# Kernel tuning notes

Hardware: AMD Instinct MI355X
Metric: run time of the kernel (lower is better)

## Reference

```python
import jax, jax.numpy as jnp
import numpy as np

B, T, E, H, C = 64, 512, 768, 128, 18


def setup_inputs() -> dict:
    key = jax.random.key(0)
    ks = jax.random.split(key, 16)
    s = 1.0 / np.sqrt(H)
    inp = {
        "x": jax.random.normal(ks[0], (B, T, E), jnp.float32),
        "attention_mask": jnp.ones((B, T), jnp.int32),
        "labels": jax.random.randint(ks[1], (B, T), 0, C, jnp.int32),
        "Wih_f": jax.random.uniform(ks[2], (4 * H, E), jnp.float32, -s, s),
        "Whh_f": jax.random.uniform(ks[3], (4 * H, H), jnp.float32, -s, s),
        "b_f": jax.random.uniform(ks[4], (4 * H,), jnp.float32, -s, s),
        "Wih_b": jax.random.uniform(ks[5], (4 * H, E), jnp.float32, -s, s),
        "Whh_b": jax.random.uniform(ks[6], (4 * H, H), jnp.float32, -s, s),
        "b_b": jax.random.uniform(ks[7], (4 * H,), jnp.float32, -s, s),
        "Wfc": jax.random.uniform(ks[8], (C, 2 * H), jnp.float32, -s, s),
        "bfc": jax.random.uniform(ks[9], (C,), jnp.float32, -s, s),
        "start_trans": jax.random.normal(ks[10], (C,), jnp.float32) * 0.1,
        "end_trans": jax.random.normal(ks[11], (C,), jnp.float32) * 0.1,
        "trans": jax.random.normal(ks[12], (C, C), jnp.float32) * 0.1,
    }
    return inp


def _lstm_dir(x, Wih, Whh, b, reverse=False):
    # x: [B, T, E] -> hidden states [B, T, H]; torch LSTM gate order i,f,g,o
    if reverse:
        x = x[:, ::-1]
    pre = jnp.einsum("bte,ge->btg", x, Wih) + b  # [B, T, 4H] input projection once
    h0 = jnp.zeros((x.shape[0], H), x.dtype)

    def step(carry, pt):
        h, c = carry
        g = pt + h @ Whh.T
        i, f, gg, o = jnp.split(g, 4, axis=-1)
        c = jax.nn.sigmoid(f) * c + jax.nn.sigmoid(i) * jnp.tanh(gg)
        h = jax.nn.sigmoid(o) * jnp.tanh(c)
        return (h, c), h

    _, hs = jax.lax.scan(step, (h0, h0), jnp.swapaxes(pre, 0, 1))
    hs = jnp.swapaxes(hs, 0, 1)
    if reverse:
        hs = hs[:, ::-1]
    return hs


def _crf_loglik(em, tags, mask, start, end, trans):
    # pytorch-crf log-likelihood, batch_first. em [B,T,C], tags/mask [B,T]
    b, t, _ = em.shape
    maskf = mask.astype(em.dtype)
    tags = tags.astype(jnp.int32)
    # numerator: score of the given tag path
    em_sc = jnp.take_along_axis(em, tags[..., None], axis=2)[..., 0]  # [B,T]
    num = start[tags[:, 0]] + em_sc[:, 0]
    num = num + jnp.sum(em_sc[:, 1:] * maskf[:, 1:], axis=1)
    num = num + jnp.sum(trans[tags[:, :-1], tags[:, 1:]] * maskf[:, 1:], axis=1)
    last_idx = jnp.sum(mask.astype(jnp.int32), axis=1) - 1
    last_tags = jnp.take_along_axis(tags, last_idx[:, None], axis=1)[:, 0]
    num = num + end[last_tags]
    # denominator: forward algorithm (logsumexp recurrence over time)
    alpha0 = start + em[:, 0]  # [B,C]

    def step(alpha, inp):
        e_t, m_t = inp
        new = jax.scipy.special.logsumexp(alpha[:, :, None] + trans[None], axis=1) + e_t
        return jnp.where(m_t[:, None], new, alpha), None

    alpha, _ = jax.lax.scan(
        step, alpha0,
        (jnp.swapaxes(em[:, 1:], 0, 1), jnp.swapaxes(mask[:, 1:].astype(bool), 0, 1)),
    )
    den = jax.scipy.special.logsumexp(alpha + end, axis=1)
    return num - den


def _viterbi(em, start, end, trans):
    # em [B,T,C] -> best path [B,T] (full mask)
    s0 = start + em[:, 0]

    def fstep(score, e_t):
        cand = score[:, :, None] + trans[None]  # [B,C,C]
        return jnp.max(cand, axis=1) + e_t, jnp.argmax(cand, axis=1)

    score, bptr = jax.lax.scan(fstep, s0, jnp.swapaxes(em[:, 1:], 0, 1))  # bptr [T-1,B,C]
    last = jnp.argmax(score + end, axis=1)  # [B]

    def bstep(tag, ptr_t):
        prev = jnp.take_along_axis(ptr_t, tag[:, None], axis=1)[:, 0]
        return prev, prev

    _, path = jax.lax.scan(bstep, last, bptr, reverse=True)  # [T-1,B]
    return jnp.concatenate([jnp.swapaxes(path, 0, 1), last[:, None]], axis=1)


def reference(x, attention_mask, labels, Wih_f, Whh_f, b_f, Wih_b, Whh_b, b_b,
              Wfc, bfc, start_trans, end_trans, trans):
    hf = _lstm_dir(x, Wih_f, Whh_f, b_f, reverse=False)
    hb = _lstm_dir(x, Wih_b, Whh_b, b_b, reverse=True)
    seq = jnp.concatenate([hf, hb], axis=-1)  # [B,T,2H]
    em = seq @ Wfc.T + bfc  # [B,T,C] emissions
    mask = attention_mask.astype(bool)
    llh = _crf_loglik(em, labels, mask, start_trans, end_trans, trans)
    loss = -jnp.sum(llh) / x.shape[0]  # reduction='sum' then / batch_size
    path = _viterbi(em, start_trans, end_trans, trans) + 1  # res_paths = x+1
    return path, loss
```

## Files before the change

### kernel.cpp

```cpp
#include <hip/hip_runtime.h>
#include <hip/hip_bf16.h>
#include <math.h>

typedef __attribute__((ext_vector_type(8))) short short8;
typedef __attribute__((ext_vector_type(4))) float f32x4;

constexpr int nB = 64, nT = 512, nE = 768, nH = 128, nG = 512, nC = 18;
constexpr int nBT = nB * nT;

__device__ __forceinline__ float bf2f(unsigned short u) { return __uint_as_float(((unsigned int)u) << 16); }
__device__ __forceinline__ unsigned short f2bf(float f) {
  __hip_bfloat16 h = __float2bfloat16(f);
  return *reinterpret_cast<unsigned short*>(&h);
}
__device__ __forceinline__ float rlane(float v, int lane) {
  return __uint_as_float(__builtin_amdgcn_readlane(__float_as_uint(v), lane));
}
__device__ __forceinline__ float fast_sig(float x) {
  return __builtin_amdgcn_rcpf(1.0f + __builtin_amdgcn_exp2f(-1.44269504f * x));
}
__device__ __forceinline__ float fast_tanh(float x) {
  return 1.0f - 2.0f * __builtin_amdgcn_rcpf(1.0f + __builtin_amdgcn_exp2f(2.88539008f * x));
}
__device__ __forceinline__ float max3h(float a, float b, float c) { return fmaxf(fmaxf(a, b), c); }

__global__ __launch_bounds__(256) void cvt_all(const float* __restrict__ x,
                                               const float* __restrict__ wF,
                                               const float* __restrict__ wB,
                                               unsigned short* __restrict__ xo,
                                               unsigned short* __restrict__ wFo,
                                               unsigned short* __restrict__ wBo) {
  const float* in; unsigned short* out; int n8, bid, nblk;
  if (blockIdx.x < 4096)      { in = x;  out = xo;  n8 = nBT * nE / 8; bid = blockIdx.x;        nblk = 4096; }
  else if (blockIdx.x < 4288) { in = wF; out = wFo; n8 = nG * nE / 8;  bid = blockIdx.x - 4096; nblk = 192; }
  else                        { in = wB; out = wBo; n8 = nG * nE / 8;  bid = blockIdx.x - 4288; nblk = 192; }
  int i = bid * 256 + threadIdx.x;
  const int stride = nblk * 256;
  for (; i < n8; i += stride) {
    const float4 a = ((const float4*)in)[(size_t)i * 2];
    const float4 b = ((const float4*)in)[(size_t)i * 2 + 1];
    unsigned short u[8] = {f2bf(a.x), f2bf(a.y), f2bf(a.z), f2bf(a.w),
                           f2bf(b.x), f2bf(b.y), f2bf(b.z), f2bf(b.w)};
    ((float4*)out)[i] = *(float4*)u;
  }
}

__global__ __launch_bounds__(256) void proj_kernel(
    const unsigned short* __restrict__ xbf,
    const unsigned short* __restrict__ wfb, const unsigned short* __restrict__ wbb,
    const float* __restrict__ biasF, const float* __restrict__ biasB,
    unsigned short* __restrict__ Pf, unsigned short* __restrict__ Pb)
{
  const int bid = blockIdx.x;
  const int mt = bid & 255, sub = bid >> 8;
  const int dir = sub >> 2, nt = sub & 3;
  const unsigned short* W = dir ? wbb : wfb;
  const float* bias = dir ? biasB : biasF;
  unsigned short* P = dir ? Pb : Pf;
  const int m0 = mt * 128, n0 = nt * 128;

  __shared__ unsigned short As[128 * 40];
  __shared__ unsigned short Bs[128 * 40];
  const int tid = threadIdx.x;
  const int w = tid >> 6, lane = tid & 63, l15 = lane & 15, l4 = lane >> 4;
  const int wr = w >> 1, wc = w & 1;
  const int srow = tid >> 1, shalf = tid & 1;

  const unsigned short* srcA = xbf + (size_t)(m0 + srow) * nE + shalf * 16;
  const unsigned short* srcB = W + (size_t)(n0 + srow) * nE + shalf * 16;

  f32x4 acc[4][4];
#pragma unroll
  for (int i = 0; i < 4; ++i)
#pragma unroll
    for (int j = 0; j < 4; ++j) acc[i][j] = (f32x4){0.f, 0.f, 0.f, 0.f};

  for (int k0 = 0; k0 < nE; k0 += 32) {
    const float4 a0 = *(const float4*)(srcA + k0);
    const float4 a1 = *(const float4*)(srcA + k0 + 8);
    const float4 b0 = *(const float4*)(srcB + k0);
    const float4 b1 = *(const float4*)(srcB + k0 + 8);
    __syncthreads();
    *(float4*)&As[srow * 40 + shalf * 16] = a0;
    *(float4*)&As[srow * 40 + shalf * 16 + 8] = a1;
    *(float4*)&Bs[srow * 40 + shalf * 16] = b0;
    *(float4*)&Bs[srow * 40 + shalf * 16 + 8] = b1;
    __syncthreads();
    short8 af[4], bfr[4];
#pragma unroll
    for (int i = 0; i < 4; ++i) af[i] = *(const short8*)&As[(wr * 64 + i * 16 + l15) * 40 + l4 * 8];
#pragma unroll
    for (int j = 0; j < 4; ++j) bfr[j] = *(const short8*)&Bs[(wc * 64 + j * 16 + l15) * 40 + l4 * 8];
#pragma unroll
    for (int i = 0; i < 4; ++i)
#pragma unroll
      for (int j = 0; j < 4; ++j)
        acc[i][j] = __builtin_amdgcn_mfma_f32_16x16x32_bf16(af[i], bfr[j], acc[i][j], 0, 0, 0);
  }
  float bv[4];
#pragma unroll
  for (int j = 0; j < 4; ++j) bv[j] = bias[n0 + wc * 64 + j * 16 + l15];
#pragma unroll
  for (int i = 0; i < 4; ++i) {
#pragma unroll
    for (int j = 0; j < 4; ++j) {
      const int col = n0 + wc * 64 + j * 16 + l15;
#pragma unroll
      for (int r = 0; r < 4; ++r) {
        const int row = m0 + wr * 64 + i * 16 + l4 * 4 + r;
        P[(size_t)row * nG + col] = f2bf(acc[i][j][r] + bv[j]);
      }
    }
  }
}

__global__ __launch_bounds__(256, 1) void lstm_kernel(
    const unsigned short* __restrict__ Pf, const unsigned short* __restrict__ Pb,
    const float* __restrict__ WhhF, const float* __restrict__ WhhB,
    unsigned short* __restrict__ hf, unsigned short* __restrict__ hb)
{
  const int bid = blockIdx.x;
  const int dir = bid & 1, pair = bid >> 1;
  const int b0 = pair * 2;
  const unsigned short* pre = dir ? Pb : Pf;
  const float* Whh = dir ? WhhB : WhhF;
  unsigned short* hout = dir ? hb : hf;

  const int tid = threadIdx.x, w = tid >> 6, lane = tid & 63;
  const int l15 = lane & 15, l4 = lane >> 4;
  const int batch = l15 & 1, msel = l15 >> 1;
  const int cell = w * 32 + msel * 4 + l4;

  __shared__ unsigned short h_lds[2 * 2 * 128];

  short8 Af[8][4];
#pragma unroll
  for (int m = 0; m < 8; ++m) {
    const int gp = w * 128 + m * 16 + l15;
    const int gorig = (gp & 3) * 128 + (gp >> 2);
#pragma unroll
    for (int kk = 0; kk < 4; ++kk) {
      const float* wp = Whh + (size_t)gorig * nH + kk * 32 + l4 * 8;
      const float4 v0 = *(const float4*)wp;
      const float4 v1 = *(const float4*)(wp + 4);
      unsigned short u[8] = {f2bf(v0.x), f2bf(v0.y), f2bf(v0.z), f2bf(v0.w),
                             f2bf(v1.x), f2bf(v1.y), f2bf(v1.z), f2bf(v1.w)};
      Af[m][kk] = *(short8*)u;
    }
  }
  for (int i = tid; i < 2 * 2 * 128; i += 256) h_lds[i] = 0;

  float c_state = 0.f;
  const unsigned short* pbase = pre + (size_t)(b0 + batch) * nT * nG + cell;

  unsigned short pA[4], pB[4];
  {
    const int tt0 = dir ? (nT - 1) : 0;
    const int tt1 = dir ? (nT - 2) : 1;
#pragma unroll
    for (int r = 0; r < 4; ++r) pA[r] = pbase[(size_t)tt0 * nG + r * 128];
#pragma unroll
    for (int r = 0; r < 4; ++r) pB[r] = pbase[(size_t)tt1 * nG + r * 128];
  }
  __syncthreads();

#define LSTM_STEP(RB, T, BUFC)                                                   \
  {                                                                              \
    const int ttime = dir ? (nT - 1 - (T)) : (T);                                \
    float pg[4];                                                                 \
    _Pragma("unroll")                                                            \
    for (int r = 0; r < 4; ++r) pg[r] = bf2f(BUFC[r]);                           \
    {                                                                            \
      const int tl = ((T) + 2 < nT) ? (T) + 2 : (T);                             \
      const int ttl = dir ? (nT - 1 - tl) : tl;                                  \
      _Pragma("unroll")                                                          \
      for (int r = 0; r < 4; ++r) BUFC[r] = pbase[(size_t)ttl * nG + r * 128];   \
    }                                                                            \
    short8 bfr[4];                                                               \
    _Pragma("unroll")                                                            \
    for (int kk = 0; kk < 4; ++kk)                                               \
      bfr[kk] = *(const short8*)&h_lds[(RB) * 256 + batch * 128 + kk * 32 + l4 * 8]; \
    f32x4 acc[8];                                                                \
    _Pragma("unroll")                                                            \
    for (int m = 0; m < 8; ++m) acc[m] = (f32x4){0.f, 0.f, 0.f, 0.f};            \
    _Pragma("unroll")                                                            \
    for (int kk = 0; kk < 4; ++kk)                                               \
      _Pragma("unroll")                                                          \
      for (int m = 0; m < 8; ++m)                                                \
        acc[m] = __builtin_amdgcn_mfma_f32_16x16x32_bf16(Af[m][kk], bfr[kk], acc[m], 0, 0, 0); \
    const f32x4 t0 = (msel & 1) ? acc[1] : acc[0];                               \
    const f32x4 t1 = (msel & 1) ? acc[3] : acc[2];                               \
    const f32x4 t2 = (msel & 1) ? acc[5] : acc[4];                               \
    const f32x4 t3 = (msel & 1) ? acc[7] : acc[6];                               \
    const f32x4 u0 = (msel & 2) ? t1 : t0;                                       \
    const f32x4 u1 = (msel & 2) ? t3 : t2;                                       \
    const f32x4 g = (msel & 4) ? u1 : u0;                                        \
    const float gi = g[0] + pg[0], gf = g[1] + pg[1], gg = g[2] + pg[2], go = g[3] + pg[3]; \
    c_state = fast_sig(gf) * c_state + fast_sig(gi) * fast_tanh(gg);             \
    const float hval = fast_sig(go) * fast_tanh(c_state);                        \
    const unsigned short hu = f2bf(hval);                                        \
    h_lds[((RB) ^ 1) * 256 + batch * 128 + cell] = hu;                           \
    hout[((size_t)(b0 + batch) * nT + ttime) * nH + cell] = hu;                  \
    asm volatile("s_waitcnt lgkmcnt(0)" ::: "memory");                           \
    __builtin_amdgcn_sched_barrier(0);                                           \
    __builtin_amdgcn_s_barrier();                                                \
  }

  for (int t2 = 0; t2 < nT; t2 += 2) {
    LSTM_STEP(0, t2, pA)
    LSTM_STEP(1, t2 + 1, pB)
  }
#undef LSTM_STEP
}

__global__ __launch_bounds__(256) void em_kernel(
    const unsigned short* __restrict__ hf, const unsigned short* __restrict__ hb,
    const float* __restrict__ Wfc, const float* __restrict__ bfc,
    float* __restrict__ em)
{
  __shared__ float seq[32][260];
  __shared__ float Wf[18][260];
  const int tid = threadIdx.x;
  const int row0 = blockIdx.x * 32;
  for (int i = tid; i < 32 * 32; i += 256) {
    const int r = i >> 5, seg = i & 31;
    const unsigned short* src = (seg < 16) ? (hf + (size_t)(row0 + r) * nH + seg * 8)
                                           : (hb + (size_t)(row0 + r) * nH + (seg - 16) * 8);
    const float4 v = *(const float4*)src;
    const unsigned short* u = (const unsigned short*)&v;
#pragma unroll
    for (int k = 0; k < 8; ++k) seq[r][seg * 8 + k] = bf2f(u[k]);
  }
  for (int i = tid; i < nC * 256; i += 256) {
    const int cc = i >> 8, k = i & 255;
    Wf[cc][k] = Wfc[cc * 256 + k];
  }
  __syncthreads();
  for (int o = tid; o < 32 * nC; o += 256) {
    const int r = o / nC, cc = o - r * nC;
    float acc = bfc[cc];
    const float4* s4 = (const float4*)&seq[r][0];
    const float4* w4 = (const float4*)&Wf[cc][0];
#pragma unroll
    for (int q = 0; q < 64; ++q) {
      const float4 a = s4[q]; const float4 wv = w4[q];
      acc += a.x * wv.x + a.y * wv.y + a.z * wv.z + a.w * wv.w;
    }
    em[(size_t)(row0 + r) * nC + cc] = acc;
  }
}

__global__ __launch_bounds__(64) void crfvit_kernel(
    const float* __restrict__ em, const int* __restrict__ labels,
    const int* __restrict__ mask, const float* __restrict__ start,
    const float* __restrict__ endt, const float* __restrict__ trans,
    float* __restrict__ llh, float* __restrict__ out_path)
{
  constexpr float K2 = 1.44269504088896f;
  constexpr float LN2 = 0.69314718055995f;
  const int b = blockIdx.x >> 1, role = blockIdx.x & 1;
  const int l = threadIdx.x;
  __shared__ float tr[nC * nC];
  __shared__ unsigned char bp[(nT - 1) * nC];
  __shared__ unsigned char path[nT];
  for (int i = l; i < nC * nC; i += 64) tr[i] = trans[i];
  __syncthreads();
  const float* eb = em + (size_t)b * nT * nC;
  const int lc = l < nC ? l : nC - 1;

#define MAX18T(c) fmaxf(max3h(max3h(c[0], c[1], c[2]), max3h(c[3], c[4], c[5]), max3h(c[6], c[7], c[8])),     \
                        max3h(max3h(c[9], c[10], c[11]), max3h(c[12], c[13], c[14]), max3h(c[15], c[16], c[17])))

  if (role == 0) {
    const int* tg = labels + (size_t)b * nT;
    const int* mk = mask + (size_t)b * nT;

    float np = 0.f; int cnt = 0;
    for (int t = l; t < nT; t += 64) {
      const int tag = tg[t];
      const float e = eb[(size_t)t * nC + tag];
      if (t == 0) np += start[tag] + e;
      else np += (float)mk[t] * (e + tr[tg[t - 1] * nC + tag]);
      cnt += mk[t];
    }
#pragma unroll
    for (int off = 32; off; off >>= 1) { np += __shfl_xor(np, off); cnt += __shfl_xor(cnt, off); }
    const float num = np + endt[tg[cnt - 1]];

    float M2[nC];
#pragma unroll
    for (int i = 0; i < nC; ++i) M2[i] = __builtin_amdgcn_exp2f(tr[i * nC + lc] * K2);

    float alpha2 = (start[lc] + eb[lc]) * K2;
    float ec[8], en[8];
#pragma unroll
    for (int j = 0; j < 8; ++j) ec[j] = eb[j * nC + lc] * K2;
#pragma unroll
    for (int j = 0; j < 8; ++j) en[j] = eb[(8 + j) * nC + lc] * K2;
    unsigned long long mb = __ballot(mk[l] != 0);

#define CRF_STEP(T, E) {                                                          \
      float A2 = alpha2;                                                          \
      A2 = fmaxf(A2, __shfl_xor(A2, 32)); A2 = fmaxf(A2, __shfl_xor(A2, 16));     \
      A2 = fmaxf(A2, __shfl_xor(A2, 8));  A2 = fmaxf(A2, __shfl_xor(A2, 4));      \
      A2 = fmaxf(A2, __shfl_xor(A2, 2));  A2 = fmaxf(A2, __shfl_xor(A2, 1));      \
      const float vv = __builtin_amdgcn_exp2f(alpha2 - A2);                       \
      float s0 = 0.f, s1 = 0.f, s2 = 0.f;                                         \
      _Pragma("unroll")                                                           \
      for (int i = 0; i < nC; i += 3) {                                           \
        s0 = fmaf(rlane(vv, i), M2[i], s0);                                       \
        s1 = fmaf(rlane(vv, i + 1), M2[i + 1], s1);                               \
        s2 = fmaf(rlane(vv, i + 2), M2[i + 2], s2);                               \
      }                                                                           \
      const float anew = A2 + __builtin_amdgcn_logf((s0 + s1) + s2) + (E);        \
      alpha2 = ((mb >> ((T) & 63)) & 1) ? anew : alpha2;                          \
    }

#pragma unroll
    for (int j = 1; j < 8; ++j) CRF_STEP(j, ec[j])
    for (int c = 1; c < 64; ++c) {
#pragma unroll
      for (int j = 0; j < 8; ++j) ec[j] = en[j];
      const int tn = (c < 63) ? (c + 1) * 8 : 504;
#pragma unroll
      for (int j = 0; j < 8; ++j) en[j] = eb[(size_t)(tn + j) * nC + lc] * K2;
      if ((c & 7) == 0) mb = __ballot(mk[c * 8 + l] != 0);
#pragma unroll
      for (int j = 0; j < 8; ++j) CRF_STEP(c * 8 + j, ec[j])
    }
#undef CRF_STEP
    const float v = (l < nC) ? (alpha2 + endt[l] * K2) : -3.0e38f;
    float m = v;
#pragma unroll
    for (int off = 32; off; off >>= 1) m = fmaxf(m, __shfl_xor(m, off));
    float s = (l < nC) ? __builtin_amdgcn_exp2f(v - m) : 0.f;
#pragma unroll
    for (int off = 32; off; off >>= 1) s += __shfl_xor(s, off);
    if (l == 0) llh[b] = num - (m + __builtin_amdgcn_logf(s)) * LN2;
  } else {
    float trc[nC];
#pragma unroll
    for (int i = 0; i < nC; ++i) trc[i] = tr[i * nC + lc];

    float score_r = start[lc] + eb[lc];
    float ec[8], en[8];
#pragma unroll
    for (int j = 0; j < 8; ++j) ec[j] = eb[j * nC + lc];
#pragma unroll
    for (int j = 0; j < 8; ++j) en[j] = eb[(8 + j) * nC + lc];

#define VIT_STEP(T, E) {                                                          \
      float cand[nC];                                                             \
      _Pragma("unroll")                                                           \
      for (int i = 0; i < nC; ++i) cand[i] = rlane(score_r, i) + trc[i];          \
      const float m = MAX18T(cand);                                               \
      int sel[nC];                                                                \
      _Pragma("unroll")                                                           \
      for (int i = 0; i < nC; ++i) sel[i] = (cand[i] == m) ? i : 63;              \
      int arg = sel[0];                                                           \
      _Pragma("unroll")                                                           \
      for (int i = 1; i < nC; ++i) arg = min(arg, sel[i]);                        \
      score_r = m + (E);                                                          \
      if (l < nC) bp[((T) - 1) * nC + l] = (unsigned char)arg;                    \
    }

#pragma unroll
    for (int j = 1; j < 8; ++j) VIT_STEP(j, ec[j])
    for (int c = 1; c < 64; ++c) {
#pragma unroll
      for (int j = 0; j < 8; ++j) ec[j] = en[j];
      const int tn = (c < 63) ? (c + 1) * 8 : 504;
#pragma unroll
      for (int j = 0; j < 8; ++j) en[j] = eb[(size_t)(tn + j) * nC + lc];
#pragma unroll
      for (int j = 0; j < 8; ++j) VIT_STEP(c * 8 + j, ec[j])
    }
#undef VIT_STEP
    if (l == 0) {
      float mm = -3.0e38f; int last = 0;
      for (int i = 0; i < nC; ++i) {
        const float v = rlane(score_r, i) + endt[i];
        if (v > mm) { mm = v; last = i; }
      }
      path[nT - 1] = (unsigned char)last;
      int cur = last;
      for (int t = nT - 2; t >= 0; --t) { cur = bp[t * nC + cur]; path[t] = (unsigned char)cur; }
    }
    asm volatile("s_waitcnt lgkmcnt(0)" ::: "memory");
    __builtin_amdgcn_wave_barrier();
    for (int t = l; t < nT; t += 64) out_path[(size_t)b * nT + t] = (float)(path[t] + 1);
  }
#undef MAX18T
}

__global__ __launch_bounds__(64) void loss_kernel(const float* __restrict__ llh, float* __restrict__ out)
{
  const int l = threadIdx.x;
  float v = llh[l];
#pragma unroll
  for (int off = 32; off; off >>= 1) v += __shfl_xor(v, off);
  if (l == 0) out[0] = -v / (float)nB;
}

extern "C" void kernel_launch(void* const* d_in, const int* in_sizes, int n_in,
                              void* d_out, int out_size, void* d_ws, size_t ws_size,
                              hipStream_t stream)
{
  const float* x      = (const float*)d_in[0];
  const int*   amask  = (const int*)d_in[1];
  const int*   labels = (const int*)d_in[2];
  const float* Wih_f  = (const float*)d_in[3];
  const float* Whh_f  = (const float*)d_in[4];
  const float* b_f    = (const float*)d_in[5];
  const float* Wih_b  = (const float*)d_in[6];
  const float* Whh_b  = (const float*)d_in[7];
  const float* b_b    = (const float*)d_in[8];
  const float* Wfc    = (const float*)d_in[9];
  const float* bfc    = (const float*)d_in[10];
  const float* start  = (const float*)d_in[11];
  const float* endt   = (const float*)d_in[12];
  const float* trans  = (const float*)d_in[13];

  float* out = (float*)d_out;
  float* ws = (float*)d_ws;
  unsigned short* preF = (unsigned short*)ws;
  unsigned short* preB = preF + (size_t)nBT * nG;
  unsigned short* hf   = preB + (size_t)nBT * nG;
  unsigned short* hb   = hf + (size_t)nBT * nH;
  float* em  = (float*)(hb + (size_t)nBT * nH);
  float* llh = em + (size_t)nBT * nC;
  unsigned short* xbf = (unsigned short*)(llh + 64);
  unsigned short* wfb = xbf + (size_t)nBT * nE;
  unsigned short* wbb = wfb + (size_t)nG * nE;

  cvt_all<<<4480, 256, 0, stream>>>(x, Wih_f, Wih_b, xbf, wfb, wbb);
  proj_kernel<<<2048, 256, 0, stream>>>(xbf, wfb, wbb, b_f, b_b, preF, preB);
  lstm_kernel<<<64, 256, 0, stream>>>(preF, preB, Whh_f, Whh_b, hf, hb);
  em_kernel<<<1024, 256, 0, stream>>>(hf, hb, Wfc, bfc, em);
  crfvit_kernel<<<128, 64, 0, stream>>>(em, labels, amask, start, endt, trans, llh, out);
  loss_kernel<<<1, 64, 0, stream>>>(llh, out + nBT);
}
```

Before: 562.6 us.

## Process four batches per LSTM block with 512 threads and fold loss into CRF kernel

Each LSTM block now handles four batch rows per direction with 8 waves, so only 32 blocks run instead of 64. Each wave does half as many MFMAs per step, and an XOR swizzle on the hidden-state LDS layout avoids bank conflicts. The separate loss reduction kernel is replaced by atomicAdd from the CRF kernel plus a memset, which saves one launch. The trade-off is a larger barrier group per time step and a non-deterministic float summation order for the loss.

```diff
diff --git a/kernel.cpp b/kernel.cpp
--- a/kernel.cpp
+++ b/kernel.cpp
@@ -114,29 +114,30 @@
   }
 }
 
-__global__ __launch_bounds__(256, 1) void lstm_kernel(
+__global__ __launch_bounds__(512, 1) void lstm_kernel(
     const unsigned short* __restrict__ Pf, const unsigned short* __restrict__ Pb,
     const float* __restrict__ WhhF, const float* __restrict__ WhhB,
     unsigned short* __restrict__ hf, unsigned short* __restrict__ hb)
 {
   const int bid = blockIdx.x;
-  const int dir = bid & 1, pair = bid >> 1;
-  const int b0 = pair * 2;
+  const int dir = bid & 1, grp = bid >> 1;
+  const int b0 = grp * 4;
   const unsigned short* pre = dir ? Pb : Pf;
   const float* Whh = dir ? WhhB : WhhF;
   unsigned short* hout = dir ? hb : hf;
 
   const int tid = threadIdx.x, w = tid >> 6, lane = tid & 63;
   const int l15 = lane & 15, l4 = lane >> 4;
-  const int batch = l15 & 1, msel = l15 >> 1;
-  const int cell = w * 32 + msel * 4 + l4;
-
-  __shared__ unsigned short h_lds[2 * 2 * 128];
-
-  short8 Af[8][4];
-#pragma unroll
-  for (int m = 0; m < 8; ++m) {
-    const int gp = w * 128 + m * 16 + l15;
+  const int batch = l15 & 3, msel = l15 >> 2;
+  const int cell = w * 16 + msel * 4 + l4;
+  const int swz = batch * 40;
+
+  __shared__ unsigned short h_lds[2 * 4 * 128];
+
+  short8 Af[4][4];
+#pragma unroll
+  for (int m = 0; m < 4; ++m) {
+    const int gp = w * 64 + m * 16 + l15;
     const int gorig = (gp & 3) * 128 + (gp >> 2);
 #pragma unroll
     for (int kk = 0; kk < 4; ++kk) {
@@ -148,7 +149,7 @@
       Af[m][kk] = *(short8*)u;
     }
   }
-  for (int i = tid; i < 2 * 2 * 128; i += 256) h_lds[i] = 0;
+  for (int i = tid; i < 2 * 4 * 128; i += 512) h_lds[i] = 0;
 
   float c_state = 0.f;
   const unsigned short* pbase = pre + (size_t)(b0 + batch) * nT * nG + cell;
@@ -178,28 +179,27 @@
     }                                                                            \
     short8 bfr[4];                                                               \
     _Pragma("unroll")                                                            \
-    for (int kk = 0; kk < 4; ++kk)                                               \
-      bfr[kk] = *(const short8*)&h_lds[(RB) * 256 + batch * 128 + kk * 32 + l4 * 8]; \
-    f32x4 acc[8];                                                                \
+    for (int kk = 0; kk < 4; ++kk) {                                             \
+      const int idx = (RB) * 512 + batch * 128 + ((kk * 32 + l4 * 8) ^ swz);     \
+      bfr[kk] = *(const short8*)&h_lds[idx];                                     \
+    }                                                                            \
+    f32x4 acc[4];                                                                \
     _Pragma("unroll")                                                            \
-    for (int m = 0; m < 8; ++m) acc[m] = (f32x4){0.f, 0.f, 0.f, 0.f};            \
+    for (int m = 0; m < 4; ++m) acc[m] = (f32x4){0.f, 0.f, 0.f, 0.f};            \
     _Pragma("unroll")                                                            \
     for (int kk = 0; kk < 4; ++kk)                                               \
       _Pragma("unroll")                                                          \
-      for (int m = 0; m < 8; ++m)                                                \
+      for (int m = 0; m < 4; ++m)                                                \
         acc[m] = __builtin_amdgcn_mfma_f32_16x16x32_bf16(Af[m][kk], bfr[kk], acc[m], 0, 0, 0); \
-    const f32x4 t0 = (msel & 1) ? acc[1] : acc[0];                               \
-    const f32x4 t1 = (msel & 1) ? acc[3] : acc[2];                               \
-    const f32x4 t2 = (msel & 1) ? acc[5] : acc[4];                               \
-    const f32x4 t3 = (msel & 1) ? acc[7] : acc[6];                               \
-    const f32x4 u0 = (msel & 2) ? t1 : t0;                                       \
-    const f32x4 u1 = (msel & 2) ? t3 : t2;                                       \
-    const f32x4 g = (msel & 4) ? u1 : u0;                                        \
-    const float gi = g[0] + pg[0], gf = g[1] + pg[1], gg = g[2] + pg[2], go = g[3] + pg[3]; \
+    const float g0 = msel < 2 ? (msel == 0 ? acc[0][0] : acc[1][0]) : (msel == 2 ? acc[2][0] : acc[3][0]); \
+    const float g1 = msel < 2 ? (msel == 0 ? acc[0][1] : acc[1][1]) : (msel == 2 ? acc[2][1] : acc[3][1]); \
+    const float g2 = msel < 2 ? (msel == 0 ? acc[0][2] : acc[1][2]) : (msel == 2 ? acc[2][2] : acc[3][2]); \
+    const float g3 = msel < 2 ? (msel == 0 ? acc[0][3] : acc[1][3]) : (msel == 2 ? acc[2][3] : acc[3][3]); \
+    const float gi = g0 + pg[0], gf = g1 + pg[1], gg = g2 + pg[2], go = g3 + pg[3]; \
     c_state = fast_sig(gf) * c_state + fast_sig(gi) * fast_tanh(gg);             \
     const float hval = fast_sig(go) * fast_tanh(c_state);                        \
     const unsigned short hu = f2bf(hval);                                        \
-    h_lds[((RB) ^ 1) * 256 + batch * 128 + cell] = hu;                           \
+    h_lds[((RB) ^ 1) * 512 + batch * 128 + (cell ^ swz)] = hu;                   \
     hout[((size_t)(b0 + batch) * nT + ttime) * nH + cell] = hu;                  \
     asm volatile("s_waitcnt lgkmcnt(0)" ::: "memory");                           \
     __builtin_amdgcn_sched_barrier(0);                                           \
@@ -254,7 +254,7 @@
     const float* __restrict__ em, const int* __restrict__ labels,
     const int* __restrict__ mask, const float* __restrict__ start,
     const float* __restrict__ endt, const float* __restrict__ trans,
-    float* __restrict__ llh, float* __restrict__ out_path)
+    float* __restrict__ loss_out, float* __restrict__ out_path)
 {
   constexpr float K2 = 1.44269504088896f;
   constexpr float LN2 = 0.69314718055995f;
@@ -336,7 +336,10 @@
     float s = (l < nC) ? __builtin_amdgcn_exp2f(v - m) : 0.f;
 #pragma unroll
     for (int off = 32; off; off >>= 1) s += __shfl_xor(s, off);
-    if (l == 0) llh[b] = num - (m + __builtin_amdgcn_logf(s)) * LN2;
+    if (l == 0) {
+      const float llh_b = num - (m + __builtin_amdgcn_logf(s)) * LN2;
+      atomicAdd(loss_out, -llh_b / (float)nB);
+    }
   } else {
     float trc[nC];
 #pragma unroll
@@ -391,15 +394,6 @@
     for (int t = l; t < nT; t += 64) out_path[(size_t)b * nT + t] = (float)(path[t] + 1);
   }
 #undef MAX18T
-}
-
-__global__ __launch_bounds__(64) void loss_kernel(const float* __restrict__ llh, float* __restrict__ out)
-{
-  const int l = threadIdx.x;
-  float v = llh[l];
-#pragma unroll
-  for (int off = 32; off; off >>= 1) v += __shfl_xor(v, off);
-  if (l == 0) out[0] = -v / (float)nB;
 }
 
 extern "C" void kernel_launch(void* const* d_in, const int* in_sizes, int n_in,
@@ -428,15 +422,15 @@
   unsigned short* hf   = preB + (size_t)nBT * nG;
   unsigned short* hb   = hf + (size_t)nBT * nH;
   float* em  = (float*)(hb + (size_t)nBT * nH);
-  float* llh = em + (size_t)nBT * nC;
-  unsigned short* xbf = (unsigned short*)(llh + 64);
+  float* pad = em + (size_t)nBT * nC;
+  unsigned short* xbf = (unsigned short*)(pad + 64);
   unsigned short* wfb = xbf + (size_t)nBT * nE;
   unsigned short* wbb = wfb + (size_t)nG * nE;
 
+  hipMemsetAsync(out + nBT, 0, sizeof(float), stream);
   cvt_all<<<4480, 256, 0, stream>>>(x, Wih_f, Wih_b, xbf, wfb, wbb);
   proj_kernel<<<2048, 256, 0, stream>>>(xbf, wfb, wbb, b_f, b_b, preF, preB);
-  lstm_kernel<<<64, 256, 0, stream>>>(preF, preB, Whh_f, Whh_b, hf, hb);
+  lstm_kernel<<<32, 512, 0, stream>>>(preF, preB, Whh_f, Whh_b, hf, hb);
   em_kernel<<<1024, 256, 0, stream>>>(hf, hb, Wfc, bfc, em);
-  crfvit_kernel<<<128, 64, 0, stream>>>(em, labels, amask, start, endt, trans, llh, out);
-  loss_kernel<<<1, 64, 0, stream>>>(llh, out + nBT);
-}
+  crfvit_kernel<<<128, 64, 0, stream>>>(em, labels, amask, start, endt, trans, out + nBT, out);
+}
```

After: 541.9 us (median of 2 runs). 1.04x faster.
